# Optimization experiments

Hardware: AMD Instinct MI355X
Metric: run time of the kernel (lower is better)

Reference implementation:

```python
import jax, jax.numpy as jnp
import numpy as np

N_NODES = 100000
N_EDGES = 1600000
IN_C, HID_C, OUT_C = 128, 128, 64


def gcn_conv(x, W, b, src, dst, n_nodes):
    """PyG-style GCNConv: h = x @ W; add self-loops; symmetric deg^-1/2 norm;
    scatter-add aggregation; + bias. Self-loop contribution added analytically
    (norm for self-loop edge i->i is deg_i^-1) instead of materializing edges."""
    h = x @ W  # [N, C_out]
    # degree over dst including self-loops (edge weights are all ones)
    deg = jax.ops.segment_sum(jnp.ones((src.shape[0],), h.dtype), dst,
                              num_segments=n_nodes) + 1.0
    dinv = jax.lax.rsqrt(deg)  # deg >= 1 always
    norm = dinv[src] * dinv[dst]  # [E]
    agg = jax.ops.segment_sum(h[src] * norm[:, None], dst, num_segments=n_nodes)
    agg = agg + h * (dinv * dinv)[:, None]  # self-loop term
    return agg + b


def setup_inputs() -> dict:
    key = jax.random.key(0)
    k0, k1, k2, k3, k4, k5 = jax.random.split(key, 6)
    x = jax.random.normal(k0, (N_NODES, IN_C), dtype=jnp.float32)
    edge_index = jax.random.randint(k1, (2, N_EDGES), 0, N_NODES, dtype=jnp.int64)
    s1 = 1.0 / np.sqrt(IN_C)
    s2 = 1.0 / np.sqrt(HID_C)
    W1 = jax.random.uniform(k2, (IN_C, HID_C), jnp.float32, -s1, s1)
    b1 = jax.random.uniform(k3, (HID_C,), jnp.float32, -s1, s1)
    W2 = jax.random.uniform(k4, (HID_C, OUT_C), jnp.float32, -s2, s2)
    b2 = jax.random.uniform(k5, (OUT_C,), jnp.float32, -s2, s2)
    return {"x": x, "W1": W1, "b1": b1, "W2": W2, "b2": b2,
            "edge_index": edge_index}


def reference(x, W1, b1, W2, b2, edge_index):
    src, dst = edge_index[0], edge_index[1]
    h = gcn_conv(x, W1, b1, src, dst, N_NODES)
    h = jax.nn.relu(h)
    out = gcn_conv(h, W2, b2, src, dst, N_NODES)
    return out
```

## Files before the change

kernel.cpp:

```cpp
#include <hip/hip_runtime.h>


static constexpr int BSHIFT = 7;
static constexpr int BWIDTH = 1 << BSHIFT;
static constexpr int MAXBUCK = 2048;
static constexpr int NPART = 256;

static constexpr size_t OFF_FLAG = 0;
static constexpr size_t OFF_DEG  = 256;
static constexpr size_t OFF_ROW  = 458752;
static constexpr size_t OFF_BSUM = 917504;
static constexpr size_t OFF_CCNT = 925696;
static constexpr size_t OFF_COFF = 937984;
static constexpr size_t OFF_DINV = 962560;
static constexpr size_t OFF_CSR  = 1376256;
static constexpr size_t OFF_HS1  = 8388608;
static constexpr size_t OFF_OUT1 = 35651584;
static constexpr size_t OFF_HS2  = 62914560;
static constexpr size_t OFF_H2   = 75714560;

__device__ __forceinline__ unsigned short f2bf(float f) {
    unsigned u = __float_as_uint(f);
    u += 0x7fffu + ((u >> 16) & 1u);
    return (unsigned short)(u >> 16);
}

typedef __attribute__((ext_vector_type(8))) short bf16x8;
typedef __attribute__((ext_vector_type(4))) float f32x4;

__global__ void detect_kernel(const unsigned* __restrict__ w,
                              unsigned* __restrict__ flag) {
    int i = blockIdx.x * blockDim.x + threadIdx.x;
    if (w[2 * i + 1] != 0u) atomicOr(flag, 1u);
}

__device__ __forceinline__ int edge_dst(const unsigned* w, unsigned flag,
                                        int e, int E) {
    return flag ? (int)w[E + e] : (int)w[2 * E + 2 * e];
}
__device__ __forceinline__ int edge_src(const unsigned* w, unsigned flag,
                                        int e, int E) {
    return flag ? (int)w[e] : (int)w[2 * e];
}

__global__ __launch_bounds__(1024) void coarse_hist_kernel(
    const unsigned* __restrict__ w, const unsigned* __restrict__ flag,
    unsigned* __restrict__ ccnt, unsigned* __restrict__ h2, int E, int nbuck) {
    __shared__ unsigned hist[MAXBUCK];
    for (int i = threadIdx.x; i < nbuck; i += 1024) hist[i] = 0;
    __syncthreads();
    const unsigned f = *flag;
    const int per = (E + gridDim.x - 1) / gridDim.x;
    const int e0 = blockIdx.x * per, e1 = min(E, e0 + per);
    for (int e = e0 + (int)threadIdx.x; e < e1; e += 1024)
        atomicAdd(&hist[edge_dst(w, f, e, E) >> BSHIFT], 1u);
    __syncthreads();
    for (int i = threadIdx.x; i < nbuck; i += 1024) {
        unsigned h = hist[i];
        h2[(size_t)i * NPART + blockIdx.x] = h;
        if (h) atomicAdd(&ccnt[i], h);
    }
}

__global__ __launch_bounds__(1024) void coarse_scan_kernel(
    const unsigned* __restrict__ ccnt, unsigned* __restrict__ coff, int nbuck) {
    __shared__ unsigned sh[1024];
    const int t = threadIdx.x;
    unsigned run = 0;
    for (int b0 = 0; b0 < nbuck; b0 += 1024) {
        unsigned v = (b0 + t < nbuck) ? ccnt[b0 + t] : 0u;
        sh[t] = v;
        __syncthreads();
        for (int off = 1; off < 1024; off <<= 1) {
            unsigned a = (t >= off) ? sh[t - off] : 0u;
            __syncthreads();
            sh[t] += a;
            __syncthreads();
        }
        if (b0 + t < nbuck) coff[b0 + t] = run + sh[t] - v;
        run += sh[1023];
        __syncthreads();
    }
    if (t == 0) coff[nbuck] = run;
}

__global__ __launch_bounds__(NPART) void off2d_kernel(
    unsigned* __restrict__ h2, const unsigned* __restrict__ coff) {
    __shared__ unsigned sh[NPART];
    const int b = blockIdx.x, t = threadIdx.x;
    unsigned v = h2[(size_t)b * NPART + t];
    sh[t] = v;
    __syncthreads();
#pragma unroll
    for (int off = 1; off < NPART; off <<= 1) {
        unsigned a = (t >= off) ? sh[t - off] : 0u;
        __syncthreads();
        sh[t] += a;
        __syncthreads();
    }
    h2[(size_t)b * NPART + t] = coff[b] + sh[t] - v;
}

__global__ __launch_bounds__(1024) void partition_kernel(
    const unsigned* __restrict__ w, const unsigned* __restrict__ flag,
    const unsigned* __restrict__ h2, unsigned* __restrict__ part, int E,
    int nbuck) {
    __shared__ unsigned lcur[MAXBUCK];
    for (int i = threadIdx.x; i < nbuck; i += 1024)
        lcur[i] = h2[(size_t)i * NPART + blockIdx.x];
    __syncthreads();
    const unsigned f = *flag;
    const int per = (E + gridDim.x - 1) / gridDim.x;
    const int e0 = blockIdx.x * per, e1 = min(E, e0 + per);
    for (int e = e0 + (int)threadIdx.x; e < e1; e += 1024) {
        int d = edge_dst(w, f, e, E);
        int s = edge_src(w, f, e, E);
        unsigned pos = atomicAdd(&lcur[d >> BSHIFT], 1u);
        part[pos] = (unsigned)s | ((unsigned)(d & (BWIDTH - 1)) << 20);
    }
}

__global__ __launch_bounds__(256) void bucket_csr_kernel(
    const unsigned* __restrict__ part, const unsigned* __restrict__ coff,
    unsigned* __restrict__ deg, int* __restrict__ csr, int N) {
    __shared__ unsigned cnt[BWIDTH];
    __shared__ unsigned sc[BWIDTH];
    __shared__ unsigned cur[BWIDTH];
    const int b = blockIdx.x, base = b << BSHIFT, t = threadIdx.x;
    if (t < BWIDTH) cnt[t] = 0;
    __syncthreads();
    const int e0 = (int)coff[b], e1 = (int)coff[b + 1];
    for (int e = e0 + t; e < e1; e += 256)
        atomicAdd(&cnt[part[e] >> 20], 1u);
    __syncthreads();
    if (t < BWIDTH && base + t < N) deg[base + t] = cnt[t];
    if (t < BWIDTH) sc[t] = cnt[t];
    __syncthreads();
#pragma unroll
    for (int off = 1; off < BWIDTH; off <<= 1) {
        unsigned a = (t < BWIDTH && t >= off) ? sc[t - off] : 0u;
        __syncthreads();
        if (t < BWIDTH) sc[t] += a;
        __syncthreads();
    }
    if (t < BWIDTH) cur[t] = (unsigned)e0 + sc[t] - cnt[t];
    __syncthreads();
    for (int e = e0 + t; e < e1; e += 256) {
        unsigned pk = part[e];
        unsigned p = atomicAdd(&cur[pk >> 20], 1u);
        csr[p] = (int)(pk & 0xFFFFFu);
    }
}

__global__ __launch_bounds__(1024) void scan1_kernel(
    const unsigned* __restrict__ deg, unsigned* __restrict__ row,
    unsigned* __restrict__ bsum, int N) {
    __shared__ unsigned sh[1024];
    int gid = blockIdx.x * 1024 + threadIdx.x;
    int t = threadIdx.x;
    unsigned v = (gid < N) ? deg[gid] : 0u;
    sh[t] = v;
    __syncthreads();
#pragma unroll
    for (int off = 1; off < 1024; off <<= 1) {
        unsigned add = (t >= off) ? sh[t - off] : 0u;
        __syncthreads();
        sh[t] += add;
        __syncthreads();
    }
    if (gid < N) row[gid + 1] = sh[t];
    if (t == 1023) bsum[blockIdx.x] = sh[1023];
}

__global__ __launch_bounds__(1024) void scan2_kernel(unsigned* __restrict__ bsum,
                                                     int NB) {
    __shared__ unsigned sh[1024];
    const int t = threadIdx.x;
    unsigned v = (t < NB) ? bsum[t] : 0u;
    sh[t] = v;
    __syncthreads();
#pragma unroll
    for (int off = 1; off < 1024; off <<= 1) {
        unsigned a = (t >= off) ? sh[t - off] : 0u;
        __syncthreads();
        sh[t] += a;
        __syncthreads();
    }
    if (t < NB) bsum[t] = sh[t] - v;
}

__global__ void scan3_kernel(unsigned* __restrict__ row,
                             const unsigned* __restrict__ bsum,
                             const unsigned* __restrict__ deg,
                             float* __restrict__ dinv, int N) {
    int gid = blockIdx.x * blockDim.x + threadIdx.x;
    if (gid >= N) return;
    row[gid + 1] += bsum[gid >> 10];
    if (gid == 0) row[0] = 0u;
    dinv[gid] = rsqrtf((float)deg[gid] + 1.0f);
}

template <int BN, bool ABF16>
__global__ __launch_bounds__(256) void gemm_mfma(
    const void* __restrict__ Av, const float* __restrict__ B,
    const float* __restrict__ dinv, unsigned short* __restrict__ out, int M) {
    constexpr int NT = BN / 16;
    __shared__ short sA[16384];
    __shared__ short sB[NT * 2048];

    const int t = threadIdx.x;
    const int row0 = blockIdx.x * 128;
    const int w = t >> 6, lane = t & 63;
    const int m = lane & 15, q = lane >> 4;

    if (ABF16) {
        const unsigned short* A = (const unsigned short*)Av;
        for (int g = t; g < 2048; g += 256) {
            int r = g >> 4, k0 = (g & 15) << 3;
            uint4 v = make_uint4(0u, 0u, 0u, 0u);
            if (row0 + r < M) v = *(const uint4*)(A + (size_t)(row0 + r) * 128 + k0);
            int off = ((((r >> 4) * 4 + (k0 >> 5)) * 16 + (r & 15)) * 4 +
                       ((k0 >> 3) & 3)) * 8;
            *(uint4*)(sA + off) = v;
        }
    } else {
        const float* A = (const float*)Av;
        for (int g = t; g < 4096; g += 256) {
            int r = g >> 5, k0 = (g & 31) << 2;
            float4 v = make_float4(0.f, 0.f, 0.f, 0.f);
            if (row0 + r < M) v = *(const float4*)(A + (size_t)(row0 + r) * 128 + k0);
            ushort4 u;
            u.x = f2bf(v.x); u.y = f2bf(v.y); u.z = f2bf(v.z); u.w = f2bf(v.w);
            int off = ((((r >> 4) * 4 + (k0 >> 5)) * 16 + (r & 15)) * 4 +
                       ((k0 >> 3) & 3)) * 8 + (k0 & 4);
            *(ushort4*)(sA + off) = u;
        }
    }
    for (int g = t; g < BN * 32; g += 256) {
        int n = g % BN, k0 = (g / BN) * 4;
        float f0 = B[(size_t)(k0 + 0) * BN + n];
        float f1 = B[(size_t)(k0 + 1) * BN + n];
        float f2 = B[(size_t)(k0 + 2) * BN + n];
        float f3 = B[(size_t)(k0 + 3) * BN + n];
        ushort4 u;
        u.x = f2bf(f0); u.y = f2bf(f1); u.z = f2bf(f2); u.w = f2bf(f3);
        int off = ((((n >> 4) * 4 + (k0 >> 5)) * 16 + (n & 15)) * 4 +
                   ((k0 >> 3) & 3)) * 8 + (k0 & 4);
        *(ushort4*)(sB + off) = u;
    }
    __syncthreads();

    f32x4 acc[2][NT];
#pragma unroll
    for (int lt = 0; lt < 2; lt++)
#pragma unroll
        for (int nt = 0; nt < NT; nt++) acc[lt][nt] = (f32x4){0.f, 0.f, 0.f, 0.f};

    const int fb = (m * 4 + q) * 8;
#pragma unroll
    for (int ks = 0; ks < 4; ks++) {
        bf16x8 a0 = *(const bf16x8*)(sA + ((w * 2 + 0) * 4 + ks) * 512 + fb);
        bf16x8 a1 = *(const bf16x8*)(sA + ((w * 2 + 1) * 4 + ks) * 512 + fb);
#pragma unroll
        for (int nt = 0; nt < NT; nt++) {
            bf16x8 b = *(const bf16x8*)(sB + (nt * 4 + ks) * 512 + fb);
            acc[0][nt] = __builtin_amdgcn_mfma_f32_16x16x32_bf16(a0, b, acc[0][nt], 0, 0, 0);
            acc[1][nt] = __builtin_amdgcn_mfma_f32_16x16x32_bf16(a1, b, acc[1][nt], 0, 0, 0);
        }
    }

#pragma unroll
    for (int lt = 0; lt < 2; lt++) {
#pragma unroll
        for (int r = 0; r < 4; r++) {
            int row = row0 + w * 32 + lt * 16 + q * 4 + r;
            if (row < M) {
                float s = dinv[row];
#pragma unroll
                for (int nt = 0; nt < NT; nt++)
                    out[(size_t)row * BN + nt * 16 + m] = f2bf(acc[lt][nt][r] * s);
            }
        }
    }
}

template <int C, bool RELU, bool OUTBF>
__global__ __launch_bounds__(256) void agg_kernel(
    const int* __restrict__ csr, const unsigned* __restrict__ row,
    const unsigned short* __restrict__ hsb, const float* __restrict__ dinv,
    const float* __restrict__ bias, void* __restrict__ outv, int N) {
    constexpr int LPN = C / 8;
    const int tid = blockIdx.x * 256 + threadIdx.x;
    const int i = tid / LPN;
    const int l = tid % LPN;
    if (i >= N) return;

    const int co = 8 * l;
    float s0 = 0.f, s1 = 0.f, s2 = 0.f, s3 = 0.f,
          s4 = 0.f, s5 = 0.f, s6 = 0.f, s7 = 0.f;
    {
        uint4 u = *(const uint4*)(hsb + (size_t)i * C + co);
        s0 += __uint_as_float(u.x << 16); s1 += __uint_as_float(u.x & 0xffff0000u);
        s2 += __uint_as_float(u.y << 16); s3 += __uint_as_float(u.y & 0xffff0000u);
        s4 += __uint_as_float(u.z << 16); s5 += __uint_as_float(u.z & 0xffff0000u);
        s6 += __uint_as_float(u.w << 16); s7 += __uint_as_float(u.w & 0xffff0000u);
    }

    const int rs = (int)row[i], re = (int)row[i + 1];
    for (int e0 = rs; e0 < re; e0 += LPN) {
        int idx = (e0 + l < re) ? csr[e0 + l] : 0;
        const int cnt = min(LPN, re - e0);
#pragma unroll 4
        for (int j = 0; j < cnt; j++) {
            int s = __shfl(idx, j, LPN);
            uint4 u = *(const uint4*)(hsb + (size_t)s * C + co);
            s0 += __uint_as_float(u.x << 16); s1 += __uint_as_float(u.x & 0xffff0000u);
            s2 += __uint_as_float(u.y << 16); s3 += __uint_as_float(u.y & 0xffff0000u);
            s4 += __uint_as_float(u.z << 16); s5 += __uint_as_float(u.z & 0xffff0000u);
            s6 += __uint_as_float(u.w << 16); s7 += __uint_as_float(u.w & 0xffff0000u);
        }
    }

    const float sc = dinv[i];
    const float4 ba = *(const float4*)(bias + co);
    const float4 bb = *(const float4*)(bias + co + 4);
    float o0 = s0 * sc + ba.x, o1 = s1 * sc + ba.y;
    float o2 = s2 * sc + ba.z, o3 = s3 * sc + ba.w;
    float o4 = s4 * sc + bb.x, o5 = s5 * sc + bb.y;
    float o6 = s6 * sc + bb.z, o7 = s7 * sc + bb.w;
    if (RELU) {
        o0 = fmaxf(o0, 0.f); o1 = fmaxf(o1, 0.f); o2 = fmaxf(o2, 0.f);
        o3 = fmaxf(o3, 0.f); o4 = fmaxf(o4, 0.f); o5 = fmaxf(o5, 0.f);
        o6 = fmaxf(o6, 0.f); o7 = fmaxf(o7, 0.f);
    }
    if (OUTBF) {
        uint4 u;
        u.x = (unsigned)f2bf(o0) | ((unsigned)f2bf(o1) << 16);
        u.y = (unsigned)f2bf(o2) | ((unsigned)f2bf(o3) << 16);
        u.z = (unsigned)f2bf(o4) | ((unsigned)f2bf(o5) << 16);
        u.w = (unsigned)f2bf(o6) | ((unsigned)f2bf(o7) << 16);
        *(uint4*)((unsigned short*)outv + (size_t)i * C + co) = u;
    } else {
        float4 a = make_float4(o0, o1, o2, o3);
        float4 b = make_float4(o4, o5, o6, o7);
        *(float4*)((float*)outv + (size_t)i * C + co) = a;
        *(float4*)((float*)outv + (size_t)i * C + co + 4) = b;
    }
}

extern "C" void kernel_launch(void* const* d_in, const int* in_sizes, int n_in,
                              void* d_out, int out_size, void* d_ws,
                              size_t ws_size, hipStream_t stream) {
    const float* x  = (const float*)d_in[0];
    const float* W1 = (const float*)d_in[1];
    const float* b1 = (const float*)d_in[2];
    const float* W2 = (const float*)d_in[3];
    const float* b2 = (const float*)d_in[4];
    const unsigned* ew = (const unsigned*)d_in[5];
    const int E = in_sizes[5] / 2;
    const int N = in_sizes[0] / 128;
    const int NB = (N + 1023) >> 10;
    const int nbuck = (N + BWIDTH - 1) >> BSHIFT;

    char* ws = (char*)d_ws;
    unsigned* flag = (unsigned*)(ws + OFF_FLAG);
    unsigned* deg  = (unsigned*)(ws + OFF_DEG);
    unsigned* row  = (unsigned*)(ws + OFF_ROW);
    unsigned* bsum = (unsigned*)(ws + OFF_BSUM);
    unsigned* ccnt = (unsigned*)(ws + OFF_CCNT);
    unsigned* coff = (unsigned*)(ws + OFF_COFF);
    float* dinv    = (float*)(ws + OFF_DINV);
    int* csr       = (int*)(ws + OFF_CSR);
    unsigned short* hs1  = (unsigned short*)(ws + OFF_HS1);
    unsigned short* out1 = (unsigned short*)(ws + OFF_OUT1);
    unsigned short* hs2  = (unsigned short*)(ws + OFF_HS2);
    unsigned* h2   = (unsigned*)(ws + OFF_H2);
    unsigned* part = (unsigned*)(ws + OFF_HS1);

    hipMemsetAsync(flag, 0, 4, stream);
    hipMemsetAsync(ccnt, 0, (size_t)(nbuck + 1) * 4, stream);

    detect_kernel<<<16, 256, 0, stream>>>(ew, flag);
    coarse_hist_kernel<<<NPART, 1024, 0, stream>>>(ew, flag, ccnt, h2, E, nbuck);
    coarse_scan_kernel<<<1, 1024, 0, stream>>>(ccnt, coff, nbuck);
    off2d_kernel<<<nbuck, NPART, 0, stream>>>(h2, coff);
    partition_kernel<<<NPART, 1024, 0, stream>>>(ew, flag, h2, part, E, nbuck);
    bucket_csr_kernel<<<nbuck, 256, 0, stream>>>(part, coff, deg, csr, N);
    scan1_kernel<<<NB, 1024, 0, stream>>>(deg, row, bsum, N);
    scan2_kernel<<<1, 1024, 0, stream>>>(bsum, NB);
    scan3_kernel<<<(N + 255) / 256, 256, 0, stream>>>(row, bsum, deg, dinv, N);

    gemm_mfma<128, false><<<(N + 127) / 128, 256, 0, stream>>>(x, W1, dinv, hs1, N);
    agg_kernel<128, true, true><<<(N * 16 + 255) / 256, 256, 0, stream>>>(
        csr, row, hs1, dinv, b1, out1, N);

    gemm_mfma<64, true><<<(N + 127) / 128, 256, 0, stream>>>(out1, W2, dinv, hs2, N);
    agg_kernel<64, false, false><<<(N * 8 + 255) / 256, 256, 0, stream>>>(
        csr, row, hs2, dinv, b2, d_out, N);
}
```

Before: 309.5 us.

## Split aggregation into column-half passes for cache locality; fold ccnt memset into detect

Each aggregation is split into two launches that each gather only half the feature columns, so the gathered working set per pass is half the size and fits better in L2/MALL. Each pass uses 16 lanes per node with narrower loads. The CSR index reads and the output writes become nontemporal. The ccnt memset is folded into detect_kernel to save one API call. In exchange the CSR indices and row offsets are read twice, there are two extra launches, and each lane issues smaller loads.

```diff
diff --git a/kernel.cpp b/kernel.cpp
--- a/kernel.cpp
+++ b/kernel.cpp
@@ -27,10 +27,14 @@
 
 typedef __attribute__((ext_vector_type(8))) short bf16x8;
 typedef __attribute__((ext_vector_type(4))) float f32x4;
+typedef __attribute__((ext_vector_type(2))) float f32x2;
+typedef __attribute__((ext_vector_type(2))) unsigned u32x2;
 
 __global__ void detect_kernel(const unsigned* __restrict__ w,
-                              unsigned* __restrict__ flag) {
+                              unsigned* __restrict__ flag,
+                              unsigned* __restrict__ ccnt, int nbuck) {
     int i = blockIdx.x * blockDim.x + threadIdx.x;
+    if (i <= nbuck) ccnt[i] = 0;
     if (w[2 * i + 1] != 0u) atomicOr(flag, 1u);
 }
 
@@ -284,67 +288,85 @@
     }
 }
 
-template <int C, bool RELU, bool OUTBF>
+__device__ __forceinline__ void acc2(float& a, float& b, unsigned u) {
+    a += __uint_as_float(u << 16);
+    b += __uint_as_float(u & 0xffff0000u);
+}
+
+template <int CTOT, int CVU, bool RELU, bool OUTBF>
 __global__ __launch_bounds__(256) void agg_kernel(
     const int* __restrict__ csr, const unsigned* __restrict__ row,
     const unsigned short* __restrict__ hsb, const float* __restrict__ dinv,
-    const float* __restrict__ bias, void* __restrict__ outv, int N) {
-    constexpr int LPN = C / 8;
+    const float* __restrict__ bias, void* __restrict__ outv, int N, int co0) {
     const int tid = blockIdx.x * 256 + threadIdx.x;
-    const int i = tid / LPN;
-    const int l = tid % LPN;
+    const int i = tid >> 4;
+    const int l = tid & 15;
     if (i >= N) return;
 
-    const int co = 8 * l;
-    float s0 = 0.f, s1 = 0.f, s2 = 0.f, s3 = 0.f,
-          s4 = 0.f, s5 = 0.f, s6 = 0.f, s7 = 0.f;
+    const int co = co0 + l * (2 * CVU);
+    const unsigned short* __restrict__ tab = hsb + co;
+    float s0 = 0.f, s1 = 0.f, s2 = 0.f, s3 = 0.f;
     {
-        uint4 u = *(const uint4*)(hsb + (size_t)i * C + co);
-        s0 += __uint_as_float(u.x << 16); s1 += __uint_as_float(u.x & 0xffff0000u);
-        s2 += __uint_as_float(u.y << 16); s3 += __uint_as_float(u.y & 0xffff0000u);
-        s4 += __uint_as_float(u.z << 16); s5 += __uint_as_float(u.z & 0xffff0000u);
-        s6 += __uint_as_float(u.w << 16); s7 += __uint_as_float(u.w & 0xffff0000u);
+        if (CVU == 2) {
+            u32x2 u = *(const u32x2*)(tab + (size_t)i * CTOT);
+            acc2(s0, s1, u.x); acc2(s2, s3, u.y);
+        } else {
+            unsigned u = *(const unsigned*)(tab + (size_t)i * CTOT);
+            acc2(s0, s1, u);
+        }
     }
 
     const int rs = (int)row[i], re = (int)row[i + 1];
-    for (int e0 = rs; e0 < re; e0 += LPN) {
-        int idx = (e0 + l < re) ? csr[e0 + l] : 0;
-        const int cnt = min(LPN, re - e0);
+    for (int e0 = rs; e0 < re; e0 += 16) {
+        int idx = (e0 + l < re) ? __builtin_nontemporal_load(csr + e0 + l) : 0;
+        const int cnt = min(16, re - e0);
 #pragma unroll 4
         for (int j = 0; j < cnt; j++) {
-            int s = __shfl(idx, j, LPN);
-            uint4 u = *(const uint4*)(hsb + (size_t)s * C + co);
-            s0 += __uint_as_float(u.x << 16); s1 += __uint_as_float(u.x & 0xffff0000u);
-            s2 += __uint_as_float(u.y << 16); s3 += __uint_as_float(u.y & 0xffff0000u);
-            s4 += __uint_as_float(u.z << 16); s5 += __uint_as_float(u.z & 0xffff0000u);
-            s6 += __uint_as_float(u.w << 16); s7 += __uint_as_float(u.w & 0xffff0000u);
+            int sr = __shfl(idx, j, 16);
+            if (CVU == 2) {
+                u32x2 u = *(const u32x2*)(tab + (size_t)sr * CTOT);
+                acc2(s0, s1, u.x); acc2(s2, s3, u.y);
+            } else {
+                unsigned u = *(const unsigned*)(tab + (size_t)sr * CTOT);
+                acc2(s0, s1, u);
+            }
         }
     }
 
     const float sc = dinv[i];
-    const float4 ba = *(const float4*)(bias + co);
-    const float4 bb = *(const float4*)(bias + co + 4);
-    float o0 = s0 * sc + ba.x, o1 = s1 * sc + ba.y;
-    float o2 = s2 * sc + ba.z, o3 = s3 * sc + ba.w;
-    float o4 = s4 * sc + bb.x, o5 = s5 * sc + bb.y;
-    float o6 = s6 * sc + bb.z, o7 = s7 * sc + bb.w;
+    float o0 = s0 * sc + bias[co + 0];
+    float o1 = s1 * sc + bias[co + 1];
+    float o2 = 0.f, o3 = 0.f;
+    if (CVU == 2) {
+        o2 = s2 * sc + bias[co + 2];
+        o3 = s3 * sc + bias[co + 3];
+    }
     if (RELU) {
-        o0 = fmaxf(o0, 0.f); o1 = fmaxf(o1, 0.f); o2 = fmaxf(o2, 0.f);
-        o3 = fmaxf(o3, 0.f); o4 = fmaxf(o4, 0.f); o5 = fmaxf(o5, 0.f);
-        o6 = fmaxf(o6, 0.f); o7 = fmaxf(o7, 0.f);
+        o0 = fmaxf(o0, 0.f); o1 = fmaxf(o1, 0.f);
+        o2 = fmaxf(o2, 0.f); o3 = fmaxf(o3, 0.f);
     }
     if (OUTBF) {
-        uint4 u;
-        u.x = (unsigned)f2bf(o0) | ((unsigned)f2bf(o1) << 16);
-        u.y = (unsigned)f2bf(o2) | ((unsigned)f2bf(o3) << 16);
-        u.z = (unsigned)f2bf(o4) | ((unsigned)f2bf(o5) << 16);
-        u.w = (unsigned)f2bf(o6) | ((unsigned)f2bf(o7) << 16);
-        *(uint4*)((unsigned short*)outv + (size_t)i * C + co) = u;
+        if (CVU == 2) {
+            u32x2 u;
+            u.x = (unsigned)f2bf(o0) | ((unsigned)f2bf(o1) << 16);
+            u.y = (unsigned)f2bf(o2) | ((unsigned)f2bf(o3) << 16);
+            __builtin_nontemporal_store(
+                u, (u32x2*)((unsigned short*)outv + (size_t)i * CTOT + co));
+        } else {
+            unsigned u = (unsigned)f2bf(o0) | ((unsigned)f2bf(o1) << 16);
+            __builtin_nontemporal_store(
+                u, (unsigned*)((unsigned short*)outv + (size_t)i * CTOT + co));
+        }
     } else {
-        float4 a = make_float4(o0, o1, o2, o3);
-        float4 b = make_float4(o4, o5, o6, o7);
-        *(float4*)((float*)outv + (size_t)i * C + co) = a;
-        *(float4*)((float*)outv + (size_t)i * C + co + 4) = b;
+        if (CVU == 2) {
+            f32x4 v = (f32x4){o0, o1, o2, o3};
+            __builtin_nontemporal_store(
+                v, (f32x4*)((float*)outv + (size_t)i * CTOT + co));
+        } else {
+            f32x2 v = (f32x2){o0, o1};
+            __builtin_nontemporal_store(
+                v, (f32x2*)((float*)outv + (size_t)i * CTOT + co));
+        }
     }
 }
 
@@ -378,9 +400,8 @@
     unsigned* part = (unsigned*)(ws + OFF_HS1);
 
     hipMemsetAsync(flag, 0, 4, stream);
-    hipMemsetAsync(ccnt, 0, (size_t)(nbuck + 1) * 4, stream);
-
-    detect_kernel<<<16, 256, 0, stream>>>(ew, flag);
+
+    detect_kernel<<<16, 256, 0, stream>>>(ew, flag, ccnt, nbuck);
     coarse_hist_kernel<<<NPART, 1024, 0, stream>>>(ew, flag, ccnt, h2, E, nbuck);
     coarse_scan_kernel<<<1, 1024, 0, stream>>>(ccnt, coff, nbuck);
     off2d_kernel<<<nbuck, NPART, 0, stream>>>(h2, coff);
@@ -390,11 +411,17 @@
     scan2_kernel<<<1, 1024, 0, stream>>>(bsum, NB);
     scan3_kernel<<<(N + 255) / 256, 256, 0, stream>>>(row, bsum, deg, dinv, N);
 
+    const int aggGrid = (N * 16 + 255) / 256;
+
     gemm_mfma<128, false><<<(N + 127) / 128, 256, 0, stream>>>(x, W1, dinv, hs1, N);
-    agg_kernel<128, true, true><<<(N * 16 + 255) / 256, 256, 0, stream>>>(
-        csr, row, hs1, dinv, b1, out1, N);
+    agg_kernel<128, 2, true, true><<<aggGrid, 256, 0, stream>>>(
+        csr, row, hs1, dinv, b1, out1, N, 0);
+    agg_kernel<128, 2, true, true><<<aggGrid, 256, 0, stream>>>(
+        csr, row, hs1, dinv, b1, out1, N, 64);
 
     gemm_mfma<64, true><<<(N + 127) / 128, 256, 0, stream>>>(out1, W2, dinv, hs2, N);
-    agg_kernel<64, false, false><<<(N * 8 + 255) / 256, 256, 0, stream>>>(
-        csr, row, hs2, dinv, b2, d_out, N);
-}
+    agg_kernel<64, 1, false, false><<<aggGrid, 256, 0, stream>>>(
+        csr, row, hs2, dinv, b2, d_out, N, 0);
+    agg_kernel<64, 1, false, false><<<aggGrid, 256, 0, stream>>>(
+        csr, row, hs2, dinv, b2, d_out, N, 32);
+}
```

Result: slower. 379.7 us (+22.7%).

## Pre-convert weights once and load GEMM operands directly from global memory

Applied to the files above, without the earlier changes.

A new small kernel converts W1 and W2 to bf16 in the MFMA fragment layout once per call, so each GEMM block no longer re-reads and re-converts the fp32 weights into shared memory. The GEMM now loads A fragments straight from global memory into registers and reads B fragments from the pre-laid-out global buffer, which removes shared memory and the block barrier. The ccnt memset is folded into detect_kernel. In exchange, A loads are strided per lane rather than coalesced tile loads, and B is re-read from L2/cache by every wave.

```diff
diff --git a/kernel.cpp b/kernel.cpp
--- a/kernel.cpp
+++ b/kernel.cpp
@@ -18,6 +18,8 @@
 static constexpr size_t OFF_OUT1 = 35651584;
 static constexpr size_t OFF_HS2  = 62914560;
 static constexpr size_t OFF_H2   = 75714560;
+static constexpr size_t OFF_W1S  = 77811712;
+static constexpr size_t OFF_W2S  = 77844480;
 
 __device__ __forceinline__ unsigned short f2bf(float f) {
     unsigned u = __float_as_uint(f);
@@ -29,8 +31,10 @@
 typedef __attribute__((ext_vector_type(4))) float f32x4;
 
 __global__ void detect_kernel(const unsigned* __restrict__ w,
-                              unsigned* __restrict__ flag) {
+                              unsigned* __restrict__ flag,
+                              unsigned* __restrict__ ccnt, int nbuck) {
     int i = blockIdx.x * blockDim.x + threadIdx.x;
+    if (i <= nbuck) ccnt[i] = 0;
     if (w[2 * i + 1] != 0u) atomicOr(flag, 1u);
 }
 
@@ -200,70 +204,77 @@
     dinv[gid] = rsqrtf((float)deg[gid] + 1.0f);
 }
 
+__global__ __launch_bounds__(256) void wprep_kernel(
+    const float* __restrict__ W1, const float* __restrict__ W2,
+    unsigned short* __restrict__ O1, unsigned short* __restrict__ O2) {
+    const float* W = blockIdx.x ? W2 : W1;
+    unsigned short* O = blockIdx.x ? O2 : O1;
+    const int BN = blockIdx.x ? 64 : 128;
+    const int total = 128 * BN / 4;
+    for (int g = threadIdx.x; g < total; g += 256) {
+        int n = g % BN, k0 = (g / BN) * 4;
+        ushort4 u;
+        u.x = f2bf(W[(size_t)(k0 + 0) * BN + n]);
+        u.y = f2bf(W[(size_t)(k0 + 1) * BN + n]);
+        u.z = f2bf(W[(size_t)(k0 + 2) * BN + n]);
+        u.w = f2bf(W[(size_t)(k0 + 3) * BN + n]);
+        int off = ((((n >> 4) * 4 + (k0 >> 5)) * 16 + (n & 15)) * 4 +
+                   ((k0 >> 3) & 3)) * 8 + (k0 & 4);
+        *(ushort4*)(O + off) = u;
+    }
+}
+
 template <int BN, bool ABF16>
 __global__ __launch_bounds__(256) void gemm_mfma(
-    const void* __restrict__ Av, const float* __restrict__ B,
+    const void* __restrict__ Av, const unsigned short* __restrict__ Bs,
     const float* __restrict__ dinv, unsigned short* __restrict__ out, int M) {
     constexpr int NT = BN / 16;
-    __shared__ short sA[16384];
-    __shared__ short sB[NT * 2048];
-
     const int t = threadIdx.x;
     const int row0 = blockIdx.x * 128;
     const int w = t >> 6, lane = t & 63;
     const int m = lane & 15, q = lane >> 4;
-
-    if (ABF16) {
-        const unsigned short* A = (const unsigned short*)Av;
-        for (int g = t; g < 2048; g += 256) {
-            int r = g >> 4, k0 = (g & 15) << 3;
-            uint4 v = make_uint4(0u, 0u, 0u, 0u);
-            if (row0 + r < M) v = *(const uint4*)(A + (size_t)(row0 + r) * 128 + k0);
-            int off = ((((r >> 4) * 4 + (k0 >> 5)) * 16 + (r & 15)) * 4 +
-                       ((k0 >> 3) & 3)) * 8;
-            *(uint4*)(sA + off) = v;
+    const int fb = (m * 4 + q) * 8;
+
+    const int r0 = row0 + (2 * w) * 16 + m;
+    const int r1 = r0 + 16;
+
+    f32x4 acc[2][NT];
+#pragma unroll
+    for (int lt = 0; lt < 2; lt++)
+#pragma unroll
+        for (int nt = 0; nt < NT; nt++) acc[lt][nt] = (f32x4){0.f, 0.f, 0.f, 0.f};
+
+#pragma unroll
+    for (int ks = 0; ks < 4; ks++) {
+        const int k0 = ks * 32 + q * 8;
+        bf16x8 a0 = (bf16x8){0, 0, 0, 0, 0, 0, 0, 0};
+        bf16x8 a1 = (bf16x8){0, 0, 0, 0, 0, 0, 0, 0};
+        if (ABF16) {
+            const unsigned short* A = (const unsigned short*)Av;
+            if (r0 < M) a0 = *(const bf16x8*)(A + (size_t)r0 * 128 + k0);
+            if (r1 < M) a1 = *(const bf16x8*)(A + (size_t)r1 * 128 + k0);
+        } else {
+            const float* A = (const float*)Av;
+            if (r0 < M) {
+                const float* p = A + (size_t)r0 * 128 + k0;
+                f32x4 lo = *(const f32x4*)p, hi = *(const f32x4*)(p + 4);
+                a0[0] = (short)f2bf(lo[0]); a0[1] = (short)f2bf(lo[1]);
+                a0[2] = (short)f2bf(lo[2]); a0[3] = (short)f2bf(lo[3]);
+                a0[4] = (short)f2bf(hi[0]); a0[5] = (short)f2bf(hi[1]);
+                a0[6] = (short)f2bf(hi[2]); a0[7] = (short)f2bf(hi[3]);
+            }
+            if (r1 < M) {
+                const float* p = A + (size_t)r1 * 128 + k0;
+                f32x4 lo = *(const f32x4*)p, hi = *(const f32x4*)(p + 4);
+                a1[0] = (short)f2bf(lo[0]); a1[1] = (short)f2bf(lo[1]);
+                a1[2] = (short)f2bf(lo[2]); a1[3] = (short)f2bf(lo[3]);
+                a1[4] = (short)f2bf(hi[0]); a1[5] = (short)f2bf(hi[1]);
+                a1[6] = (short)f2bf(hi[2]); a1[7] = (short)f2bf(hi[3]);
+            }
         }
-    } else {
-        const float* A = (const float*)Av;
-        for (int g = t; g < 4096; g += 256) {
-            int r = g >> 5, k0 = (g & 31) << 2;
-            float4 v = make_float4(0.f, 0.f, 0.f, 0.f);
-            if (row0 + r < M) v = *(const float4*)(A + (size_t)(row0 + r) * 128 + k0);
-            ushort4 u;
-            u.x = f2bf(v.x); u.y = f2bf(v.y); u.z = f2bf(v.z); u.w = f2bf(v.w);
-            int off = ((((r >> 4) * 4 + (k0 >> 5)) * 16 + (r & 15)) * 4 +
-                       ((k0 >> 3) & 3)) * 8 + (k0 & 4);
-            *(ushort4*)(sA + off) = u;
-        }
-    }
-    for (int g = t; g < BN * 32; g += 256) {
-        int n = g % BN, k0 = (g / BN) * 4;
-        float f0 = B[(size_t)(k0 + 0) * BN + n];
-        float f1 = B[(size_t)(k0 + 1) * BN + n];
-        float f2 = B[(size_t)(k0 + 2) * BN + n];
-        float f3 = B[(size_t)(k0 + 3) * BN + n];
-        ushort4 u;
-        u.x = f2bf(f0); u.y = f2bf(f1); u.z = f2bf(f2); u.w = f2bf(f3);
-        int off = ((((n >> 4) * 4 + (k0 >> 5)) * 16 + (n & 15)) * 4 +
-                   ((k0 >> 3) & 3)) * 8 + (k0 & 4);
-        *(ushort4*)(sB + off) = u;
-    }
-    __syncthreads();
-
-    f32x4 acc[2][NT];
-#pragma unroll
-    for (int lt = 0; lt < 2; lt++)
-#pragma unroll
-        for (int nt = 0; nt < NT; nt++) acc[lt][nt] = (f32x4){0.f, 0.f, 0.f, 0.f};
-
-    const int fb = (m * 4 + q) * 8;
-#pragma unroll
-    for (int ks = 0; ks < 4; ks++) {
-        bf16x8 a0 = *(const bf16x8*)(sA + ((w * 2 + 0) * 4 + ks) * 512 + fb);
-        bf16x8 a1 = *(const bf16x8*)(sA + ((w * 2 + 1) * 4 + ks) * 512 + fb);
 #pragma unroll
         for (int nt = 0; nt < NT; nt++) {
-            bf16x8 b = *(const bf16x8*)(sB + (nt * 4 + ks) * 512 + fb);
+            bf16x8 b = *(const bf16x8*)(Bs + (nt * 4 + ks) * 512 + fb);
             acc[0][nt] = __builtin_amdgcn_mfma_f32_16x16x32_bf16(a0, b, acc[0][nt], 0, 0, 0);
             acc[1][nt] = __builtin_amdgcn_mfma_f32_16x16x32_bf16(a1, b, acc[1][nt], 0, 0, 0);
         }
@@ -375,12 +386,15 @@
     unsigned short* out1 = (unsigned short*)(ws + OFF_OUT1);
     unsigned short* hs2  = (unsigned short*)(ws + OFF_HS2);
     unsigned* h2   = (unsigned*)(ws + OFF_H2);
+    unsigned short* w1s  = (unsigned short*)(ws + OFF_W1S);
+    unsigned short* w2s  = (unsigned short*)(ws + OFF_W2S);
     unsigned* part = (unsigned*)(ws + OFF_HS1);
 
     hipMemsetAsync(flag, 0, 4, stream);
-    hipMemsetAsync(ccnt, 0, (size_t)(nbuck + 1) * 4, stream);
-
-    detect_kernel<<<16, 256, 0, stream>>>(ew, flag);
+
+    wprep_kernel<<<2, 256, 0, stream>>>(W1, W2, w1s, w2s);
+
+    detect_kernel<<<16, 256, 0, stream>>>(ew, flag, ccnt, nbuck);
     coarse_hist_kernel<<<NPART, 1024, 0, stream>>>(ew, flag, ccnt, h2, E, nbuck);
     coarse_scan_kernel<<<1, 1024, 0, stream>>>(ccnt, coff, nbuck);
     off2d_kernel<<<nbuck, NPART, 0, stream>>>(h2, coff);
@@ -390,11 +404,11 @@
     scan2_kernel<<<1, 1024, 0, stream>>>(bsum, NB);
     scan3_kernel<<<(N + 255) / 256, 256, 0, stream>>>(row, bsum, deg, dinv, N);
 
-    gemm_mfma<128, false><<<(N + 127) / 128, 256, 0, stream>>>(x, W1, dinv, hs1, N);
+    gemm_mfma<128, false><<<(N + 127) / 128, 256, 0, stream>>>(x, w1s, dinv, hs1, N);
     agg_kernel<128, true, true><<<(N * 16 + 255) / 256, 256, 0, stream>>>(
         csr, row, hs1, dinv, b1, out1, N);
 
-    gemm_mfma<64, true><<<(N + 127) / 128, 256, 0, stream>>>(out1, W2, dinv, hs2, N);
+    gemm_mfma<64, true><<<(N + 127) / 128, 256, 0, stream>>>(out1, w2s, dinv, hs2, N);
     agg_kernel<64, false, false><<<(N * 8 + 255) / 256, 256, 0, stream>>>(
         csr, row, hs2, dinv, b2, d_out, N);
 }
```

After: 305.7 us. No clear change (-1.3%).
